# Optimization experiments

Hardware: AMD Instinct MI355X
Metric: run time of the kernel (lower is better)

Reference implementation:

```python
import jax, jax.numpy as jnp
import numpy as np
from jax import lax

B = 2048


def setup_inputs() -> dict:
    key = jax.random.key(0)
    ks = jax.random.split(key, 12)
    r = lambda k, s, sc=0.05: jax.random.normal(k, s, jnp.float32) * sc
    return {
        "w": jax.random.normal(ks[0], (B, 512), jnp.float32),
        "init_const": r(ks[1], (1, 512, 4, 4), 0.1),
        "init_conv_w": r(ks[2], (256, 512, 3, 3)),
        "init_conv_b": r(ks[3], (256,)),
        "aff1_w": r(ks[4], (256, 512)),
        "aff1_b": r(ks[5], (256,)),
        "conv1_w": r(ks[6], (128, 256, 3, 3)),
        "conv1_b": r(ks[7], (128,)),
        "aff2_w": r(ks[8], (128, 512)),
        "aff2_b": r(ks[9], (128,)),
        "conv2_w": r(ks[10], (64, 128, 3, 3)),
        "conv2_b": r(ks[11], (64,)),
    }


def _conv3(x, W):
    # 3x3 conv, stride 1, padding 1, NCHW / OIHW
    return lax.conv_general_dilated(x, W, (1, 1), ((1, 1), (1, 1)),
                                    dimension_numbers=("NCHW", "OIHW", "NCHW"))


def _lrelu(x):
    return jnp.where(x >= 0, x, 0.2 * x)


def reference(w, init_const, init_conv_w, init_conv_b,
              aff1_w, aff1_b, conv1_w, conv1_b,
              aff2_w, aff2_b, conv2_w, conv2_b):
    batch = w.shape[0]
    x = _conv3(init_const, init_conv_w) + init_conv_b[None, :, None, None]
    x = _lrelu(x)                                   # [1,256,4,4]
    x = jnp.broadcast_to(x, (batch,) + x.shape[1:])  # repeat over batch
    layers = ((aff1_w, aff1_b, conv1_w, conv1_b),
              (aff2_w, aff2_b, conv2_w, conv2_b))
    for aw, ab, cw, cb in layers:
        b_, c, h, wd = x.shape
        # bilinear upsample x2 (half-pixel centers == torch align_corners=False)
        x = jax.image.resize(x, (b_, c, 2 * h, 2 * wd), "bilinear")
        style = w @ aw.T + ab                        # [B, Cin]
        # modulated conv: conv(s*x, W) * demod, where
        # demod[b,o] = rsqrt(sum_{c,k} (s[b,c] W[o,c,k])^2 + 1e-8)
        xm = x * style[:, :, None, None]
        y = _conv3(xm, cw)                           # [B, Cout, 2h, 2w]
        w2 = jnp.sum(cw * cw, axis=(2, 3))           # [Cout, Cin]
        demod = lax.rsqrt(jnp.einsum("bc,oc->bo", style * style, w2) + 1e-8)
        x = _lrelu(y * demod[:, :, None, None] + cb[None, :, None, None])
    return x
```

## Files before the change

### kernel.cpp

```cpp
#include <hip/hip_runtime.h>
#include <hip/hip_fp16.h>

typedef _Float16 f16x8 __attribute__((ext_vector_type(8)));
typedef float f32x4 __attribute__((ext_vector_type(4)));

#define WS_X0U   0
#define WS_GHP   65536
#define WS_W2P   4259840
#define WS_WH    4407296
#define WS_AFTH  6504448
#define WS_W2TH  6897664
#define WS_S1P   7045120
#define WS_S2H   8093696
#define WS_SSQ   8617984
#define WS_D1    10190848
#define WS_D2    11239424
#define WS_X1T   11763712

__device__ __forceinline__ void up_wi(int j, int S, int& i0, int& i1,
                                      float& w0, float& w1) {
  int m = j >> 1;
  if (j & 1) { i0 = m; i1 = (m + 1 < S) ? m + 1 : S - 1; w0 = 0.75f; w1 = 0.25f; }
  else       { i0 = (m - 1 >= 0) ? m - 1 : 0; i1 = m;     w0 = 0.25f; w1 = 0.75f; }
}

__global__ __launch_bounds__(256) void k_init(const float* __restrict__ ic,
    const float* __restrict__ w0c, const float* __restrict__ b0,
    float* __restrict__ x0u) {
  int o = blockIdx.x, t = threadIdx.x;
  int pix = t & 15, cg = t >> 4;
  int py = pix >> 2, px = pix & 3;
  __shared__ float part[16][17];
  __shared__ float x4[16];
  float acc = 0.f;
  int c0 = cg * 32;
  for (int c = c0; c < c0 + 32; ++c) {
    const float* wp = w0c + (o * 512 + c) * 9;
    const float* xp = ic + c * 16;
#pragma unroll
    for (int dy = 0; dy < 3; ++dy) {
      int iy = py + dy - 1;
      if ((unsigned)iy >= 4u) continue;
#pragma unroll
      for (int dx = 0; dx < 3; ++dx) {
        int ix = px + dx - 1;
        if ((unsigned)ix >= 4u) continue;
        acc += wp[dy * 3 + dx] * xp[iy * 4 + ix];
      }
    }
  }
  part[cg][pix] = acc;
  __syncthreads();
  if (t < 16) {
    float v = b0[o];
#pragma unroll
    for (int g = 0; g < 16; ++g) v += part[g][t];
    x4[t] = (v >= 0.f) ? v : 0.2f * v;
  }
  __syncthreads();
  if (t < 64) {
    int oy = t >> 3, ox = t & 7;
    int y0, y1, xx0, xx1; float wy0, wy1, wx0, wx1;
    up_wi(oy, 4, y0, y1, wy0, wy1);
    up_wi(ox, 4, xx0, xx1, wx0, wx1);
    float v = wy0 * (wx0 * x4[y0 * 4 + xx0] + wx1 * x4[y0 * 4 + xx1])
            + wy1 * (wx0 * x4[y1 * 4 + xx0] + wx1 * x4[y1 * 4 + xx1]);
    x0u[o * 64 + t] = v;
  }
}

__global__ __launch_bounds__(256) void k_prep(const float* __restrict__ w1c,
    const float* __restrict__ x0u, _Float16* __restrict__ Ghp) {
  int o = blockIdx.x, pg = blockIdx.y, t = threadIdx.x;
  __shared__ _Float16 x0l[256][66];
  for (int i = t; i < 256 * 64; i += 256) {
    int c = i >> 6, p = i & 63;
    x0l[c][p] = (_Float16)x0u[i];
  }
  __syncthreads();
  int c = t;
  float wr9[9];
#pragma unroll
  for (int k = 0; k < 9; ++k) wr9[k] = w1c[(o * 256 + c) * 9 + k];
  int cpart = ((((c >> 3) & 3) * 16 + (o & 15)) * 8) + (c & 7);
  int cq = c >> 5, oq = o >> 4;
  for (int p = pg * 16; p < pg * 16 + 16; ++p) {
    int py = p >> 3, px = p & 7;
    float acc = 0.f;
#pragma unroll
    for (int dy = 0; dy < 3; ++dy) {
      int iy = py + dy - 1;
      if ((unsigned)iy >= 8u) continue;
#pragma unroll
      for (int dx = 0; dx < 3; ++dx) {
        int ix = px + dx - 1;
        if ((unsigned)ix >= 8u) continue;
        acc += wr9[dy * 3 + dx] * (float)x0l[c][iy * 8 + ix];
      }
    }
    Ghp[((p * 8 + oq) * 8 + cq) * 512 + cpart] = (_Float16)acc;
  }
}

__global__ __launch_bounds__(256) void k_misc(const float* __restrict__ w1c,
    const float* __restrict__ w2c, const float* __restrict__ a1w,
    const float* __restrict__ a2w, const float* __restrict__ wsrc,
    _Float16* __restrict__ w2p, _Float16* __restrict__ wh,
    _Float16* __restrict__ afTh, _Float16* __restrict__ W2Th) {
  int idx = blockIdx.x * 256 + threadIdx.x;
  if (idx < 73728) {
    int tap = idx / 8192, r = idx & 8191;
    int kg = r >> 11, mf = (r >> 9) & 3, l = (r >> 3) & 63, j = r & 7;
    int o = mf * 16 + (l & 15);
    int c = kg * 32 + (l >> 4) * 8 + j;
    w2p[idx] = (_Float16)w2c[(o * 128 + c) * 9 + tap];
  } else if (idx < 73728 + 1048576) {
    int i = idx - 73728;
    wh[i] = (_Float16)wsrc[i];
  } else if (idx < 73728 + 1048576 + 196608) {
    int i = idx - 73728 - 1048576;
    afTh[i] = (_Float16)((i < 131072) ? a1w[i] : a2w[i - 131072]);
  } else if (idx < 73728 + 1048576 + 196608 + 73728) {
    int i = idx - 73728 - 1048576 - 196608;
    int o = i / 384, k = i - o * 384;
    float v = 0.f;
    const float* wp = nullptr;
    if (o < 128 && k < 256)        wp = w1c + (o * 256 + k) * 9;
    else if (o >= 128 && k >= 256) wp = w2c + ((o - 128) * 128 + (k - 256)) * 9;
    if (wp) {
#pragma unroll
      for (int q = 0; q < 9; ++q) v += wp[q] * wp[q];
    }
    W2Th[i] = (_Float16)v;
  }
}

__global__ __launch_bounds__(256) void k_sty(const _Float16* __restrict__ wh,
    const _Float16* __restrict__ afTh, const float* __restrict__ a1b,
    const float* __restrict__ a2b, _Float16* __restrict__ s1p,
    _Float16* __restrict__ s2h, _Float16* __restrict__ ssq) {
  int t = threadIdx.x, lane = t & 63, w = t >> 6;
  int wr = w >> 1, wc = w & 1;
  int b0 = blockIdx.y * 64 + wr * 32;
  int f0 = blockIdx.x * 64 + wc * 32;
  f32x4 acc[2][2] = {};
  int lr = lane & 15, lk = (lane >> 4) * 8;
#pragma unroll
  for (int kg = 0; kg < 16; ++kg) {
    f16x8 af[2], bf[2];
#pragma unroll
    for (int mf = 0; mf < 2; ++mf)
      af[mf] = *(const f16x8*)(wh + (b0 + mf * 16 + lr) * 512 + kg * 32 + lk);
#pragma unroll
    for (int nf = 0; nf < 2; ++nf)
      bf[nf] = *(const f16x8*)(afTh + (f0 + nf * 16 + lr) * 512 + kg * 32 + lk);
#pragma unroll
    for (int mf = 0; mf < 2; ++mf)
#pragma unroll
      for (int nf = 0; nf < 2; ++nf)
        acc[mf][nf] = __builtin_amdgcn_mfma_f32_16x16x32_f16(af[mf], bf[nf], acc[mf][nf], 0, 0, 0);
  }
  int r4 = lane >> 4;
#pragma unroll
  for (int nf = 0; nf < 2; ++nf) {
    int f = f0 + nf * 16 + lr;
    float bias = (f < 256) ? a1b[f] : a2b[f - 256];
#pragma unroll
    for (int mf = 0; mf < 2; ++mf) {
#pragma unroll
      for (int r = 0; r < 4; ++r) {
        int b = b0 + mf * 16 + r4 * 4 + r;
        float v = acc[mf][nf][r] + bias;
        ssq[b * 384 + f] = (_Float16)(v * v);
        if (f < 256) {
          int flat = (((b >> 4) * 8 + (f >> 5)) * 64 + ((f >> 3) & 3) * 16 + (b & 15)) * 8 + (f & 7);
          s1p[flat] = (_Float16)v;
        } else {
          s2h[b * 128 + (f - 256)] = (_Float16)v;
        }
      }
    }
  }
}

__global__ __launch_bounds__(256) void k_dmd(const _Float16* __restrict__ ssq,
    const _Float16* __restrict__ W2Th, float* __restrict__ d1,
    float* __restrict__ d2) {
  int t = threadIdx.x, lane = t & 63, w = t >> 6;
  int wr = w >> 1, wc = w & 1;
  int b0 = blockIdx.y * 64 + wr * 32;
  int o0 = blockIdx.x * 64 + wc * 32;
  int kbeg = (blockIdx.x == 2) ? 8 : 0;
  int kend = (blockIdx.x == 2) ? 12 : 8;
  f32x4 acc[2][2] = {};
  int lr = lane & 15, lk = (lane >> 4) * 8;
  for (int kg = kbeg; kg < kend; ++kg) {
    f16x8 af[2], bf[2];
#pragma unroll
    for (int mf = 0; mf < 2; ++mf)
      af[mf] = *(const f16x8*)(ssq + (b0 + mf * 16 + lr) * 384 + kg * 32 + lk);
#pragma unroll
    for (int nf = 0; nf < 2; ++nf)
      bf[nf] = *(const f16x8*)(W2Th + (o0 + nf * 16 + lr) * 384 + kg * 32 + lk);
#pragma unroll
    for (int mf = 0; mf < 2; ++mf)
#pragma unroll
      for (int nf = 0; nf < 2; ++nf)
        acc[mf][nf] = __builtin_amdgcn_mfma_f32_16x16x32_f16(af[mf], bf[nf], acc[mf][nf], 0, 0, 0);
  }
  int r4 = lane >> 4;
#pragma unroll
  for (int mf = 0; mf < 2; ++mf) {
#pragma unroll
    for (int r = 0; r < 4; ++r) {
      int b = b0 + mf * 16 + r4 * 4 + r;
#pragma unroll
      for (int nf = 0; nf < 2; ++nf) {
        int o = o0 + nf * 16 + lr;
        float v = rsqrtf(acc[mf][nf][r] + 1e-8f);
        if (o < 128) d1[b * 128 + o] = v;
        else         d2[b * 64 + (o - 128)] = v;
      }
    }
  }
}

__global__ __launch_bounds__(256) void k_l1(const _Float16* __restrict__ s1p,
    const _Float16* __restrict__ Ghp, const float* __restrict__ d1,
    const float* __restrict__ c1b, const _Float16* __restrict__ s2h,
    __half* __restrict__ x1t) {
  int t = threadIdx.x, lane = t & 63, w = t >> 6;
  int wr = w >> 1, wc = w & 1;
  int bq0 = blockIdx.y * 8 + wr * 4;
  int nq0 = blockIdx.x * 8 + wc * 4;
  f32x4 acc[4][4] = {};
#pragma unroll
  for (int kg = 0; kg < 8; ++kg) {
    f16x8 af[4], bf[4];
#pragma unroll
    for (int mf = 0; mf < 4; ++mf)
      af[mf] = *(const f16x8*)(s1p + (((bq0 + mf) * 8 + kg) * 64 + lane) * 8);
#pragma unroll
    for (int nf = 0; nf < 4; ++nf)
      bf[nf] = *(const f16x8*)(Ghp + (((nq0 + nf) * 8 + kg) * 64 + lane) * 8);
#pragma unroll
    for (int mf = 0; mf < 4; ++mf)
#pragma unroll
      for (int nf = 0; nf < 4; ++nf)
        acc[mf][nf] = __builtin_amdgcn_mfma_f32_16x16x32_f16(af[mf], bf[nf], acc[mf][nf], 0, 0, 0);
  }
  int nc = lane & 15, r4 = lane >> 4;
#pragma unroll
  for (int mf = 0; mf < 4; ++mf) {
#pragma unroll
    for (int r = 0; r < 4; ++r) {
      int b = (bq0 + mf) * 16 + r4 * 4 + r;
#pragma unroll
      for (int nf = 0; nf < 4; ++nf) {
        int n = (nq0 + nf) * 16 + nc;
        int o = n & 127, p = n >> 7;
        float v = acc[mf][nf][r] * d1[b * 128 + o] + c1b[o];
        v = (v >= 0.f) ? v : 0.2f * v;
        v *= (float)s2h[b * 128 + o];
        x1t[(b * 64 + p) * 128 + o] = (__half)v;
      }
    }
  }
}

__global__ __launch_bounds__(256, 2) void k_l2(const __half* __restrict__ x1t,
    const float* __restrict__ d2g, const _Float16* __restrict__ w2p,
    const float* __restrict__ c2b, float* __restrict__ out) {
  int b = blockIdx.x, t = threadIdx.x;
  int lane = t & 63, w = t >> 6;
  __shared__ unsigned short xup[306 * 64];
  __shared__ unsigned short x1l[64 * 128];
  const __half* xb = x1t + b * 8192;

  for (int idx = t; idx < 1024; idx += 256) {
    int q = idx >> 4, gc = idx & 15;
    f16x8 v = *(const f16x8*)(xb + q * 128 + gc * 8);
    int gs = (gc & 8) | ((gc ^ q) & 7);
    *(f16x8*)&x1l[q * 128 + gs * 8] = v;
  }
  {
    f16x8 z = {};
    for (int idx = t; idx < 400; idx += 256) {
      int pix, g;
      if (idx < 144) { pix = 288 + (idx >> 3); g = idx & 7; }
      else {
        int j = idx - 144;
        int r = j >> 4, side = (j >> 3) & 1;
        g = j & 7;
        pix = r * 18 + side * 17;
      }
      *(f16x8*)&xup[pix * 64 + g * 8] = z;
    }
  }
  f16x8 afb[3][4];
#pragma unroll
  for (int mf = 0; mf < 4; ++mf) {
    afb[0][mf] = *(const f16x8*)(w2p + (((0 * 4 + 0) * 4 + mf) * 64 + lane) * 8);
    afb[1][mf] = *(const f16x8*)(w2p + (((1 * 4 + 0) * 4 + mf) * 64 + lane) * 8);
  }
  int fy = t >> 4, fx = t & 15;
  int y0, y1, x0, x1i; float wy0, wy1, wx0, wx1;
  up_wi(fy, 8, y0, y1, wy0, wy1);
  up_wi(fx, 8, x0, x1i, wx0, wx1);
  _Float16 wA = (_Float16)(wy0 * wx0), wB = (_Float16)(wy0 * wx1);
  _Float16 wC = (_Float16)(wy1 * wx0), wD = (_Float16)(wy1 * wx1);
  int pixb = fy * 18 + fx + 1;
  int q00 = y0 * 8 + x0, q01 = y0 * 8 + x1i, q10 = y1 * 8 + x0, q11 = y1 * 8 + x1i;
  __syncthreads();

  f32x4 acc[4][4] = {};
  f16x8 bfb[2][4];

#pragma unroll
  for (int h = 0; h < 2; ++h) {
    if (h) __syncthreads();
#pragma unroll
    for (int i = 0; i < 8; ++i) {
      int gc = h * 8 + i;
      f16x8 va = *(const f16x8*)&x1l[q00 * 128 + ((gc & 8) | ((gc ^ q00) & 7)) * 8];
      f16x8 vb = *(const f16x8*)&x1l[q01 * 128 + ((gc & 8) | ((gc ^ q01) & 7)) * 8];
      f16x8 vc = *(const f16x8*)&x1l[q10 * 128 + ((gc & 8) | ((gc ^ q10) & 7)) * 8];
      f16x8 vd = *(const f16x8*)&x1l[q11 * 128 + ((gc & 8) | ((gc ^ q11) & 7)) * 8];
      f16x8 v = va * wA;
      v += vb * wB;
      v += vc * wC;
      v += vd * wD;
      *(f16x8*)&xup[pixb * 64 + ((i ^ (pixb & 7)) * 8)] = v;
    }
    __syncthreads();
    {
      int g = 0 * 4 + (lane >> 4);
#pragma unroll
      for (int nf = 0; nf < 4; ++nf) {
        int fr = w * 4 + nf - 1;
        int srow = ((unsigned)fr < 16u) ? fr : 16;
        int pix = srow * 18 + (lane & 15);
        bfb[0][nf] = *(const f16x8*)&xup[pix * 64 + ((g ^ (pix & 7)) * 8)];
      }
    }
#pragma unroll
    for (int s = 0; s < 18; ++s) {
      const int S = h * 18 + s;
      if (s < 17) {
        int sn = s + 1, kkn = sn / 9, tapn = sn - kkn * 9;
        int dyn = tapn / 3, dxn = tapn - dyn * 3;
        int g = kkn * 4 + (lane >> 4);
#pragma unroll
        for (int nf = 0; nf < 4; ++nf) {
          int fr = w * 4 + nf + dyn - 1;
          int srow = ((unsigned)fr < 16u) ? fr : 16;
          int pix = srow * 18 + (lane & 15) + dxn;
          bfb[(s + 1) & 1][nf] = *(const f16x8*)&xup[pix * 64 + ((g ^ (pix & 7)) * 8)];
        }
      }
      if (S < 34) {
        int Sn = S + 2;
        int hn = Sn / 18, sn = Sn - hn * 18;
        int kkn = sn / 9, tapn = sn - kkn * 9;
        int kgn = hn * 2 + kkn;
#pragma unroll
        for (int mf = 0; mf < 4; ++mf)
          afb[Sn % 3][mf] = *(const f16x8*)(w2p + (((tapn * 4 + kgn) * 4 + mf) * 64 + lane) * 8);
      }
      __builtin_amdgcn_s_setprio(1);
#pragma unroll
      for (int mf = 0; mf < 4; ++mf)
#pragma unroll
        for (int nf = 0; nf < 4; ++nf)
          acc[mf][nf] = __builtin_amdgcn_mfma_f32_16x16x32_f16(afb[S % 3][mf], bfb[s & 1][nf], acc[mf][nf], 0, 0, 0);
      __builtin_amdgcn_s_setprio(0);
    }
  }
  int px = lane & 15, r4 = lane >> 4;
#pragma unroll
  for (int mf = 0; mf < 4; ++mf) {
#pragma unroll
    for (int r = 0; r < 4; ++r) {
      int o = mf * 16 + r4 * 4 + r;
      float dm = d2g[b * 64 + o], bias = c2b[o];
#pragma unroll
      for (int nf = 0; nf < 4; ++nf) {
        int py = w * 4 + nf;
        float v = acc[mf][nf][r] * dm + bias;
        v = (v >= 0.f) ? v : 0.2f * v;
        out[(b * 64 + o) * 256 + py * 16 + px] = v;
      }
    }
  }
}

extern "C" void kernel_launch(void* const* d_in, const int* in_sizes, int n_in,
                              void* d_out, int out_size, void* d_ws, size_t ws_size,
                              hipStream_t stream) {
  const float* w    = (const float*)d_in[0];
  const float* ic   = (const float*)d_in[1];
  const float* w0c  = (const float*)d_in[2];
  const float* b0   = (const float*)d_in[3];
  const float* a1w  = (const float*)d_in[4];
  const float* a1b  = (const float*)d_in[5];
  const float* w1c  = (const float*)d_in[6];
  const float* c1b  = (const float*)d_in[7];
  const float* a2w  = (const float*)d_in[8];
  const float* a2b  = (const float*)d_in[9];
  const float* w2c  = (const float*)d_in[10];
  const float* c2b  = (const float*)d_in[11];
  float* out = (float*)d_out;
  char* ws = (char*)d_ws;

  float*    x0u  = (float*)(ws + WS_X0U);
  _Float16* Ghp  = (_Float16*)(ws + WS_GHP);
  _Float16* w2p  = (_Float16*)(ws + WS_W2P);
  _Float16* wh   = (_Float16*)(ws + WS_WH);
  _Float16* afTh = (_Float16*)(ws + WS_AFTH);
  _Float16* W2Th = (_Float16*)(ws + WS_W2TH);
  _Float16* s1p  = (_Float16*)(ws + WS_S1P);
  _Float16* s2h  = (_Float16*)(ws + WS_S2H);
  _Float16* ssq  = (_Float16*)(ws + WS_SSQ);
  float*    d1   = (float*)(ws + WS_D1);
  float*    d2   = (float*)(ws + WS_D2);
  __half*   x1t  = (__half*)(ws + WS_X1T);

  k_init <<<256, 256, 0, stream>>>(ic, w0c, b0, x0u);
  dim3 gp(128, 4);
  k_prep <<<gp, 256, 0, stream>>>(w1c, x0u, Ghp);
  k_misc <<<5440, 256, 0, stream>>>(w1c, w2c, a1w, a2w, w, w2p, wh, afTh, W2Th);
  dim3 gs(6, 32);
  k_sty  <<<gs, 256, 0, stream>>>(wh, afTh, a1b, a2b, s1p, s2h, ssq);
  dim3 gd(3, 32);
  k_dmd  <<<gd, 256, 0, stream>>>(ssq, W2Th, d1, d2);
  dim3 g1(64, 16);
  k_l1   <<<g1, 256, 0, stream>>>(s1p, Ghp, d1, c1b, s2h, x1t);
  k_l2   <<<2048, 256, 0, stream>>>(x1t, d2, w2p, c2b, out);
}
```

Before: 157.7 us.

## Double-buffer upsampled tile in quarter-channel chunks and overlap build with MFMA

The layer-2 kernel now splits the 128 input channels into four 32-channel quarters held in two alternating LDS buffers with a new swizzled layout. It builds the next quarter's bilinear-upsampled tile in slices between the MFMA steps of the current quarter. Previously it built a full half, synchronised, and then computed. The aim is to hide upsampling and LDS-write latency behind tensor-core work and cut exposed barrier stalls. The cost is more barriers (one per quarter), more complex indexing, and possible register pressure from the interleaved build code.

Measured after the change: 156.0 us. No clear change (-1.0%).

```diff
diff --git a/kernel.cpp b/kernel.cpp
--- a/kernel.cpp
+++ b/kernel.cpp
@@ -22,6 +22,10 @@
   int m = j >> 1;
   if (j & 1) { i0 = m; i1 = (m + 1 < S) ? m + 1 : S - 1; w0 = 0.75f; w1 = 0.25f; }
   else       { i0 = (m - 1 >= 0) ? m - 1 : 0; i1 = m;     w0 = 0.25f; w1 = 0.75f; }
+}
+
+__device__ __forceinline__ int xq_off(int pix, int i) {
+  return (pix >> 1) * 64 + (((((pix & 1) << 2) + i) ^ ((pix >> 1) & 7)) << 3);
 }
 
 __global__ __launch_bounds__(256) void k_init(const float* __restrict__ ic,
@@ -273,7 +277,7 @@
     const float* __restrict__ c2b, float* __restrict__ out) {
   int b = blockIdx.x, t = threadIdx.x;
   int lane = t & 63, w = t >> 6;
-  __shared__ unsigned short xup[306 * 64];
+  __shared__ unsigned short xq[2][9792];
   __shared__ unsigned short x1l[64 * 128];
   const __half* xb = x1t + b * 8192;
 
@@ -286,15 +290,12 @@
   {
     f16x8 z = {};
     for (int idx = t; idx < 400; idx += 256) {
-      int pix, g;
-      if (idx < 144) { pix = 288 + (idx >> 3); g = idx & 7; }
-      else {
-        int j = idx - 144;
-        int r = j >> 4, side = (j >> 3) & 1;
-        g = j & 7;
-        pix = r * 18 + side * 17;
-      }
-      *(f16x8*)&xup[pix * 64 + g * 8] = z;
+      int pg = idx >> 3, g = idx & 7;
+      int buf = g >> 2, i = g & 3;
+      int pix;
+      if (pg < 18) pix = 288 + pg;
+      else { int j = pg - 18; pix = (j >> 1) * 18 + (j & 1) * 17; }
+      *(f16x8*)&xq[buf][xq_off(pix, i)] = z;
     }
   }
   f16x8 afb[3][4];
@@ -311,62 +312,61 @@
   _Float16 wC = (_Float16)(wy1 * wx0), wD = (_Float16)(wy1 * wx1);
   int pixb = fy * 18 + fx + 1;
   int q00 = y0 * 8 + x0, q01 = y0 * 8 + x1i, q10 = y1 * 8 + x0, q11 = y1 * 8 + x1i;
+
+  auto build_granule = [&](int qn, int i) {
+    int gc = qn * 4 + i;
+    f16x8 va = *(const f16x8*)&x1l[q00 * 128 + ((gc & 8) | ((gc ^ q00) & 7)) * 8];
+    f16x8 vb = *(const f16x8*)&x1l[q01 * 128 + ((gc & 8) | ((gc ^ q01) & 7)) * 8];
+    f16x8 vc = *(const f16x8*)&x1l[q10 * 128 + ((gc & 8) | ((gc ^ q10) & 7)) * 8];
+    f16x8 vd = *(const f16x8*)&x1l[q11 * 128 + ((gc & 8) | ((gc ^ q11) & 7)) * 8];
+    f16x8 v = va * wA;
+    v += vb * wB;
+    v += vc * wC;
+    v += vd * wD;
+    *(f16x8*)&xq[qn & 1][xq_off(pixb, i)] = v;
+  };
+
+  __syncthreads();
+#pragma unroll
+  for (int i = 0; i < 4; ++i) build_granule(0, i);
   __syncthreads();
 
   f32x4 acc[4][4] = {};
   f16x8 bfb[2][4];
-
-#pragma unroll
-  for (int h = 0; h < 2; ++h) {
-    if (h) __syncthreads();
-#pragma unroll
-    for (int i = 0; i < 8; ++i) {
-      int gc = h * 8 + i;
-      f16x8 va = *(const f16x8*)&x1l[q00 * 128 + ((gc & 8) | ((gc ^ q00) & 7)) * 8];
-      f16x8 vb = *(const f16x8*)&x1l[q01 * 128 + ((gc & 8) | ((gc ^ q01) & 7)) * 8];
-      f16x8 vc = *(const f16x8*)&x1l[q10 * 128 + ((gc & 8) | ((gc ^ q10) & 7)) * 8];
-      f16x8 vd = *(const f16x8*)&x1l[q11 * 128 + ((gc & 8) | ((gc ^ q11) & 7)) * 8];
-      f16x8 v = va * wA;
-      v += vb * wB;
-      v += vc * wC;
-      v += vd * wD;
-      *(f16x8*)&xup[pixb * 64 + ((i ^ (pixb & 7)) * 8)] = v;
-    }
-    __syncthreads();
-    {
-      int g = 0 * 4 + (lane >> 4);
-#pragma unroll
-      for (int nf = 0; nf < 4; ++nf) {
-        int fr = w * 4 + nf - 1;
-        int srow = ((unsigned)fr < 16u) ? fr : 16;
-        int pix = srow * 18 + (lane & 15);
-        bfb[0][nf] = *(const f16x8*)&xup[pix * 64 + ((g ^ (pix & 7)) * 8)];
-      }
-    }
-#pragma unroll
-    for (int s = 0; s < 18; ++s) {
-      const int S = h * 18 + s;
-      if (s < 17) {
-        int sn = s + 1, kkn = sn / 9, tapn = sn - kkn * 9;
+  int ig = lane >> 4;
+
+#pragma unroll
+  for (int q = 0; q < 4; ++q) {
+#pragma unroll
+    for (int nf = 0; nf < 4; ++nf) {
+      int fr = w * 4 + nf - 1;
+      int srow = ((unsigned)fr < 16u) ? fr : 16;
+      int pix = srow * 18 + (lane & 15);
+      bfb[0][nf] = *(const f16x8*)&xq[q & 1][xq_off(pix, ig)];
+    }
+#pragma unroll
+    for (int s = 0; s < 9; ++s) {
+      const int S = q * 9 + s;
+      if (s < 8) {
+        int tapn = s + 1;
         int dyn = tapn / 3, dxn = tapn - dyn * 3;
-        int g = kkn * 4 + (lane >> 4);
 #pragma unroll
         for (int nf = 0; nf < 4; ++nf) {
           int fr = w * 4 + nf + dyn - 1;
           int srow = ((unsigned)fr < 16u) ? fr : 16;
           int pix = srow * 18 + (lane & 15) + dxn;
-          bfb[(s + 1) & 1][nf] = *(const f16x8*)&xup[pix * 64 + ((g ^ (pix & 7)) * 8)];
+          bfb[(s + 1) & 1][nf] = *(const f16x8*)&xq[q & 1][xq_off(pix, ig)];
         }
       }
       if (S < 34) {
         int Sn = S + 2;
-        int hn = Sn / 18, sn = Sn - hn * 18;
-        int kkn = sn / 9, tapn = sn - kkn * 9;
-        int kgn = hn * 2 + kkn;
+        int qn2 = Sn / 9, tapn = Sn - qn2 * 9;
 #pragma unroll
         for (int mf = 0; mf < 4; ++mf)
-          afb[Sn % 3][mf] = *(const f16x8*)(w2p + (((tapn * 4 + kgn) * 4 + mf) * 64 + lane) * 8);
-      }
+          afb[Sn % 3][mf] = *(const f16x8*)(w2p + (((tapn * 4 + qn2) * 4 + mf) * 64 + lane) * 8);
+      }
+      if (q < 3 && (s & 1) && s < 8)
+        build_granule(q + 1, (s - 1) >> 1);
       __builtin_amdgcn_s_setprio(1);
 #pragma unroll
       for (int mf = 0; mf < 4; ++mf)
@@ -375,6 +375,7 @@
           acc[mf][nf] = __builtin_amdgcn_mfma_f32_16x16x32_f16(afb[S % 3][mf], bfb[s & 1][nf], acc[mf][nf], 0, 0, 0);
       __builtin_amdgcn_s_setprio(0);
     }
+    if (q < 3) __syncthreads();
   }
   int px = lane & 15, r4 = lane >> 4;
 #pragma unroll
```
